# Kernel optimization log

Hardware: AMD Instinct MI355X
Metric: run time of the kernel (lower is better)

## Reference

```python
import jax, jax.numpy as jnp
import numpy as np

H, W = 512, 512
CHUNK = 128            # gaussians blended per scan step
BLUR = 0.3             # antialiasing dilation (as in 3DGS EWA low-pass)
ALPHA_MIN = 1.0 / 255.0
ALPHA_MAX = 0.99


def setup_inputs() -> dict:
    key = jax.random.key(0)
    k = jax.random.split(key, 6)
    N = 8192
    means2D = jax.random.uniform(k[0], (N, 2), jnp.float32) * jnp.array([W, H], jnp.float32)
    colors = jax.random.uniform(k[1], (N, 3), jnp.float32)
    opacities = jax.random.uniform(k[2], (N, 1), jnp.float32)
    scales = jax.random.uniform(k[3], (N, 2), jnp.float32) * 15.0 + 1.0   # pixels
    rotations = jax.random.uniform(k[4], (N, 1), jnp.float32) * (2.0 * np.pi)
    depths = jax.random.uniform(k[5], (N,), jnp.float32)
    background = jnp.zeros((3,), jnp.float32)
    return dict(means2D=means2D, colors=colors, opacities=opacities,
                scales=scales, rotations=rotations, depths=depths,
                background=background)


def _rasterize(means2D, colors, opacities, scales, rotations, depths, background):
    # depth sort: front (small depth) first
    order = jnp.argsort(depths)
    m = means2D[order]                 # [N,2] (x,y)
    col = colors[order]                # [N,3]
    op = opacities[order][:, 0]        # [N]
    s = scales[order]                  # [N,2]
    th = rotations[order][:, 0]        # [N]

    # 2D covariance  Sigma = R diag(s^2) R^T
    c, si = jnp.cos(th), jnp.sin(th)
    sx2, sy2 = s[:, 0] ** 2, s[:, 1] ** 2
    A = c * c * sx2 + si * si * sy2
    Cc = si * si * sx2 + c * c * sy2
    B = c * si * (sx2 - sy2)
    det = A * Cc - B * B
    # antialiasing: dilate covariance, compensate opacity
    A2, C2 = A + BLUR, Cc + BLUR
    det2 = A2 * C2 - B * B
    op = op * jnp.sqrt(jnp.maximum(det / det2, 0.0))
    invdet = 1.0 / det2
    ia, ib, ic = C2 * invdet, -B * invdet, A2 * invdet   # Sigma^-1 entries

    # pixel centers
    ys, xs = jnp.meshgrid(jnp.arange(H, dtype=jnp.float32) + 0.5,
                          jnp.arange(W, dtype=jnp.float32) + 0.5, indexing='ij')

    N = m.shape[0]
    nchunk = N // CHUNK
    chunk = lambda a: a.reshape((nchunk, CHUNK) + a.shape[1:])
    gs = (chunk(m), chunk(col), chunk(op), chunk(ia), chunk(ib), chunk(ic))

    def step(carry, g):
        T, acc = carry                       # T:[H,W] transmittance, acc:[3,H,W]
        gm, gcol, gop, gia, gib, gic = g     # per-chunk [C,...]
        dx = xs[None] - gm[:, 0, None, None]                 # [C,H,W]
        dy = ys[None] - gm[:, 1, None, None]
        power = (-0.5 * (gia[:, None, None] * dx * dx + gic[:, None, None] * dy * dy)
                 - gib[:, None, None] * dx * dy)
        alpha = jnp.minimum(ALPHA_MAX, gop[:, None, None] * jnp.exp(power))
        alpha = jnp.where(alpha < ALPHA_MIN, 0.0, alpha)     # skip tiny splats (as CUDA)
        one_m = 1.0 - alpha
        cum = jnp.cumprod(one_m, axis=0)                     # inclusive
        Twithin = jnp.concatenate([jnp.ones_like(cum[:1]), cum[:-1]], 0)  # exclusive
        w = alpha * Twithin * T[None]                        # blend weight per gaussian
        acc = acc + jnp.einsum('nc,nhw->chw', gcol, w)
        T = T * cum[-1]
        return (T, acc), None

    init = (jnp.ones((H, W), jnp.float32), jnp.zeros((3, H, W), jnp.float32))
    (T, acc), _ = jax.lax.scan(step, init, gs)
    color = acc + background[:, None, None] * T[None]        # [3,H,W]
    return color


def reference(means2D, colors, opacities, scales, rotations, depths, background):
    return _rasterize(means2D, colors, opacities, scales, rotations, depths, background)
```

## Files before the change

kernel.cpp:

```cpp
#include <hip/hip_runtime.h>
#include <hip/hip_fp16.h>
#include <stdint.h>

#define HH 512
#define WW 512
#define NPIX (HH*WW)
#define ALPHA_MIN_C (1.0f/255.0f)
#define ALPHA_MAX_C 0.99f
#define BLUR_C 0.3f
#define TERM_EPS 1.0e-4f
#define LOG2E 1.4426950408889634f

#define JSL 512
__global__ __launch_bounds__(256) void rank_kernel(const float* __restrict__ depths,
                                                   int N, int* __restrict__ partial) {
    __shared__ uint32_t sk[JSL];
    const int tid = threadIdx.x;
    const int ngb = N >> 8;
    const int gb = blockIdx.x % ngb;
    const int jb = blockIdx.x / ngb;
    const int j0 = jb * JSL;
    for (int i = tid; i < JSL; i += 256)
        sk[i] = __float_as_uint(depths[j0 + i]);
    __syncthreads();
    const int g = gb * 256 + tid;
    const uint32_t mb = __float_as_uint(depths[g]);
    const int glim = g - j0;
    int cnt = 0;
    const uint4* sk4 = (const uint4*)sk;
#pragma unroll 8
    for (int q = 0; q < JSL / 4; ++q) {
        uint4 v = sk4[q];
        const int i4 = q * 4;
        cnt += (v.x < mb) || (v.x == mb && (i4 + 0) < glim);
        cnt += (v.y < mb) || (v.y == mb && (i4 + 1) < glim);
        cnt += (v.z < mb) || (v.z == mb && (i4 + 2) < glim);
        cnt += (v.w < mb) || (v.w == mb && (i4 + 3) < glim);
    }
    partial[jb * N + g] = cnt;
}

__global__ __launch_bounds__(256) void prep_kernel(
    const float* __restrict__ means, const float* __restrict__ colors,
    const float* __restrict__ ops, const float* __restrict__ scales,
    const float* __restrict__ rots, const int* __restrict__ partial, int N,
    float4* __restrict__ pP, float4* __restrict__ pQ) {
    int g = blockIdx.x * 256 + threadIdx.x;
    if (g >= N) return;
    int pos = 0;
#pragma unroll
    for (int s = 0; s < 16; ++s) pos += partial[s * N + g];
    float mx = means[2*g], my = means[2*g+1];
    float th = rots[g];
    float c = cosf(th), si = sinf(th);
    float sx = scales[2*g], sy = scales[2*g+1];
    float sx2 = sx*sx, sy2 = sy*sy;
    float A  = c*c*sx2 + si*si*sy2;
    float Cc = si*si*sx2 + c*c*sy2;
    float B  = c*si*(sx2 - sy2);
    float det = A*Cc - B*B;
    float A2 = A + BLUR_C, C2 = Cc + BLUR_C;
    float det2 = A2*C2 - B*B;
    float op = ops[g] * sqrtf(fmaxf(det/det2, 0.0f));
    float invd = 1.0f/det2;
    float ia = C2*invd, ib = -B*invd, ic = A2*invd;
    float iaF = -0.5f*LOG2E*ia, icF = -0.5f*LOG2E*ic, ibF = -LOG2E*ib;
    float mid = 0.5f*(A2+C2);
    float lam = mid + sqrtf(fmaxf(mid*mid - det2, 0.0f));
    float r2;
    if (op < ALPHA_MIN_C) {
        r2 = -1.0f;
    } else {
        float t = __logf(op * 255.0f);
        r2 = fmaxf(2.0f * lam * t, 0.0f) * 1.0001f + 0.25f;
    }
    __half2 h2 = __floats2half2_rn(ibF, icF);
    unsigned ibic; __builtin_memcpy(&ibic, &h2, 4);
    unsigned r10 = __float2uint_rn(fminf(colors[3*g  ], 1.0f) * 1023.0f);
    unsigned g10 = __float2uint_rn(fminf(colors[3*g+1], 1.0f) * 1023.0f);
    unsigned b10 = __float2uint_rn(fminf(colors[3*g+2], 1.0f) * 1023.0f);
    unsigned rgb = r10 | (g10 << 10) | (b10 << 20);
    pP[pos] = make_float4(mx, my, r2, op);
    pQ[pos] = make_float4(iaF, __uint_as_float(ibic), __uint_as_float(rgb), 0.0f);
}

#define NSEG 8
#define SEGG 1024
#define CHK  128
#define NCHK (SEGG/CHK)

__device__ __forceinline__ uint2 packAT(float r, float g, float b, float t) {
    __half2 hrg = __floats2half2_rn(r, g);
    __half2 hbt = __floats2half2_rn(b, t);
    uint2 u;
    __builtin_memcpy(&u.x, &hrg, 4);
    __builtin_memcpy(&u.y, &hbt, 4);
    return u;
}

__global__ __launch_bounds__(64) void seg_blend_kernel(
    const float4* __restrict__ pP, const float4* __restrict__ pQ,
    uint2* __restrict__ segbuf) {
    __shared__ __align__(16) float sG[2][CHK*8];
    const int lane = threadIdx.x;
    const int tile = blockIdx.x & 1023;
    const int seg  = blockIdx.x >> 10;
    const int tX = tile & 31, tY = tile >> 5;
    const int px = tX*16 + (lane & 15);
    const int py = tY*16 + (lane >> 4);
    const float fx = px + 0.5f, fy = py + 0.5f;
    const float x0 = tX*16 + 0.5f, x1 = x0 + 15.0f;
    const float y0 = tY*16 + 0.5f, y1 = y0 + 15.0f;
    const uint64_t lm = (1ull << lane) - 1ull;
    float T0=1.f,T1=1.f,T2=1.f,T3=1.f;
    float aR0=0.f,aG0=0.f,aB0=0.f;
    float aR1=0.f,aG1=0.f,aB1=0.f;
    float aR2=0.f,aG2=0.f,aB2=0.f;
    float aR3=0.f,aG3=0.f,aB3=0.f;
    const int gb = seg * SEGG;

    float4 a0 = pP[gb+lane],    q0 = pQ[gb+lane];
    float4 a1 = pP[gb+64+lane], q1 = pQ[gb+64+lane];
    int cntA = 0, cntB = 0;
    {
        float nx = fminf(fmaxf(a0.x,x0),x1)-a0.x, ny = fminf(fmaxf(a0.y,y0),y1)-a0.y;
        bool f0 = (nx*nx + ny*ny) <= a0.z;
        nx = fminf(fmaxf(a1.x,x0),x1)-a1.x; ny = fminf(fmaxf(a1.y,y0),y1)-a1.y;
        bool f1 = (nx*nx + ny*ny) <= a1.z;
        uint64_t m0 = __ballot(f0);
        if (f0) { float* rec = &sG[0][__popcll(m0 & lm)*8];
                  *(float4*)rec = make_float4(a0.x,a0.y,q0.x,q0.y);
                  *(float2*)(rec+4) = make_float2(a0.w,q0.z); }
        int c0 = (int)__popcll(m0);
        uint64_t m1 = __ballot(f1);
        if (f1) { float* rec = &sG[0][(c0 + __popcll(m1 & lm))*8];
                  *(float4*)rec = make_float4(a1.x,a1.y,q1.x,q1.y);
                  *(float2*)(rec+4) = make_float2(a1.w,q1.z); }
        cntA = c0 + (int)__popcll(m1);
    }
    {   const int g = gb + CHK + lane;
        a0 = pP[g]; q0 = pQ[g]; a1 = pP[g+64]; q1 = pQ[g+64]; }

    int cur = 0;
    for (int k = 0; k < NCHK; ++k) {
        const int nxt = cur ^ 1;
        if (k + 1 < NCHK) {
            float nx = fminf(fmaxf(a0.x,x0),x1)-a0.x, ny = fminf(fmaxf(a0.y,y0),y1)-a0.y;
            bool f0 = (nx*nx + ny*ny) <= a0.z;
            nx = fminf(fmaxf(a1.x,x0),x1)-a1.x; ny = fminf(fmaxf(a1.y,y0),y1)-a1.y;
            bool f1 = (nx*nx + ny*ny) <= a1.z;
            uint64_t m0 = __ballot(f0);
            if (f0) { float* rec = &sG[nxt][__popcll(m0 & lm)*8];
                      *(float4*)rec = make_float4(a0.x,a0.y,q0.x,q0.y);
                      *(float2*)(rec+4) = make_float2(a0.w,q0.z); }
            int c0 = (int)__popcll(m0);
            uint64_t m1 = __ballot(f1);
            if (f1) { float* rec = &sG[nxt][(c0 + __popcll(m1 & lm))*8];
                      *(float4*)rec = make_float4(a1.x,a1.y,q1.x,q1.y);
                      *(float2*)(rec+4) = make_float2(a1.w,q1.z); }
            const int cn = c0 + (int)__popcll(m1);
            if (nxt == 0) cntA = cn; else cntB = cn;
            if (k + 2 < NCHK) {
                const int g = gb + (k+2)*CHK + lane;
                a0 = pP[g]; q0 = pQ[g]; a1 = pP[g+64]; q1 = pQ[g+64];
            }
        }
        const int cnt = (cur == 0) ? cntA : cntB;
        const float* segp = sG[cur];
        for (int i = 0; i < cnt; ++i) {
            const float4 r0 = *(const float4*)(segp + i*8);
            const float2 r1 = *(const float2*)(segp + i*8 + 4);
            float dx = fx - r0.x;
            float dy = fy - r0.y;
            unsigned hh = __float_as_uint(r0.w);
            __half2 h2; __builtin_memcpy(&h2, &hh, 4);
            float ibv = __half2float(h2.x);
            float icv = __half2float(h2.y);
            float bse = r0.z * (dx*dx);
            float pb  = ibv * dx;
            float d1 = dy + 4.0f, d2 = dy + 8.0f, d3 = dy + 12.0f;
            float p0 = fmaf(icv, dy*dy, fmaf(pb, dy, bse));
            float p1 = fmaf(icv, d1*d1, fmaf(pb, d1, bse));
            float p2 = fmaf(icv, d2*d2, fmaf(pb, d2, bse));
            float p3 = fmaf(icv, d3*d3, fmaf(pb, d3, bse));
            float al0 = fminf(ALPHA_MAX_C, r1.x * exp2f(p0));
            float al1 = fminf(ALPHA_MAX_C, r1.x * exp2f(p1));
            float al2 = fminf(ALPHA_MAX_C, r1.x * exp2f(p2));
            float al3 = fminf(ALPHA_MAX_C, r1.x * exp2f(p3));
            al0 = (al0 >= ALPHA_MIN_C) ? al0 : 0.0f;
            al1 = (al1 >= ALPHA_MIN_C) ? al1 : 0.0f;
            al2 = (al2 >= ALPHA_MIN_C) ? al2 : 0.0f;
            al3 = (al3 >= ALPHA_MIN_C) ? al3 : 0.0f;
            if (__any((al0 > 0.f) | (al1 > 0.f) | (al2 > 0.f) | (al3 > 0.f))) {
                unsigned rgb = __float_as_uint(r1.y);
                float cr = (float)(rgb & 1023u)         * (1.0f/1023.0f);
                float cg = (float)((rgb >> 10) & 1023u) * (1.0f/1023.0f);
                float cb = (float)((rgb >> 20) & 1023u) * (1.0f/1023.0f);
                float s0 = al0*T0, s1 = al1*T1, s2 = al2*T2, s3 = al3*T3;
                aR0 = fmaf(cr,s0,aR0); aG0 = fmaf(cg,s0,aG0); aB0 = fmaf(cb,s0,aB0);
                aR1 = fmaf(cr,s1,aR1); aG1 = fmaf(cg,s1,aG1); aB1 = fmaf(cb,s1,aB1);
                aR2 = fmaf(cr,s2,aR2); aG2 = fmaf(cg,s2,aG2); aB2 = fmaf(cb,s2,aB2);
                aR3 = fmaf(cr,s3,aR3); aG3 = fmaf(cg,s3,aG3); aB3 = fmaf(cb,s3,aB3);
                T0 = fmaf(-al0,T0,T0); T1 = fmaf(-al1,T1,T1);
                T2 = fmaf(-al2,T2,T2); T3 = fmaf(-al3,T3,T3);
            }
        }
        if (__all((T0 < TERM_EPS) & (T1 < TERM_EPS) &
                  (T2 < TERM_EPS) & (T3 < TERM_EPS))) break;
        cur = nxt;
    }
    const int pix0 = py*WW + px;
    uint2* sb = segbuf + seg * NPIX;
    sb[pix0        ] = packAT(aR0, aG0, aB0, T0);
    sb[pix0 +  4*WW] = packAT(aR1, aG1, aB1, T1);
    sb[pix0 +  8*WW] = packAT(aR2, aG2, aB2, T2);
    sb[pix0 + 12*WW] = packAT(aR3, aG3, aB3, T3);
}

__global__ __launch_bounds__(256) void composite_kernel(
    const uint2* __restrict__ segbuf, const float* __restrict__ bg,
    float* __restrict__ out) {
    const int pix = blockIdx.x * 256 + threadIdx.x;
    float R = 0.f, G = 0.f, B = 0.f, T = 1.f;
#pragma unroll
    for (int s = 0; s < NSEG; ++s) {
        uint2 v = segbuf[s * NPIX + pix];
        __half2 hrg, hbt;
        __builtin_memcpy(&hrg, &v.x, 4);
        __builtin_memcpy(&hbt, &v.y, 4);
        R = fmaf(T, __half2float(hrg.x), R);
        G = fmaf(T, __half2float(hrg.y), G);
        B = fmaf(T, __half2float(hbt.x), B);
        T *= __half2float(hbt.y);
    }
    out[pix]          = R + bg[0]*T;
    out[pix +   NPIX] = G + bg[1]*T;
    out[pix + 2*NPIX] = B + bg[2]*T;
}

extern "C" void kernel_launch(void* const* d_in, const int* in_sizes, int n_in,
                              void* d_out, int out_size, void* d_ws, size_t ws_size,
                              hipStream_t stream) {
    const float* means   = (const float*)d_in[0];
    const float* colors  = (const float*)d_in[1];
    const float* ops     = (const float*)d_in[2];
    const float* scales  = (const float*)d_in[3];
    const float* rots    = (const float*)d_in[4];
    const float* depths  = (const float*)d_in[5];
    const float* bg      = (const float*)d_in[6];
    const int N = in_sizes[0] / 2;

    char* ws = (char*)d_ws;
    float4* pP    = (float4*)(ws);
    float4* pQ    = (float4*)(ws + (size_t)N*16);
    int*    part  = (int*)  (ws + (size_t)N*32);
    uint2*  segb  = (uint2*)(ws + (size_t)N*32 + (size_t)16*N*4);

    const int ngb = N / 256;
    const int njb = N / JSL;
    rank_kernel<<<dim3(ngb*njb), dim3(256), 0, stream>>>(depths, N, part);
    prep_kernel<<<dim3((N+255)/256), dim3(256), 0, stream>>>(
        means, colors, ops, scales, rots, part, N, pP, pQ);
    seg_blend_kernel<<<dim3(NSEG*1024), dim3(64), 0, stream>>>(pP, pQ, segb);
    composite_kernel<<<dim3(NPIX/256), dim3(256), 0, stream>>>(
        segb, bg, (float*)d_out);
}
```

Before: 136.6 us.

## Use per-axis ellipse bounding box culling and fold log-opacity into exponent

The preprocess now stores per-axis half-extents of the alpha-threshold ellipse instead of a circular radius from the largest eigenvalue. The tile test becomes an axis-aligned box overlap, which is tighter for elongated or rotated splats and so sends fewer gaussians to the per-pixel blend loop. Log2 of opacity is folded into the exponent so each of the four alpha evaluations loses a multiply, and the blend loop is unrolled by two. The tighter bound depends on the half-extent formula being conservative; if it is not, visible splats could be culled.

```diff
diff --git a/kernel.cpp b/kernel.cpp
--- a/kernel.cpp
+++ b/kernel.cpp
@@ -65,14 +65,14 @@
     float invd = 1.0f/det2;
     float ia = C2*invd, ib = -B*invd, ic = A2*invd;
     float iaF = -0.5f*LOG2E*ia, icF = -0.5f*LOG2E*ic, ibF = -LOG2E*ib;
-    float mid = 0.5f*(A2+C2);
-    float lam = mid + sqrtf(fmaxf(mid*mid - det2, 0.0f));
-    float r2;
+    float bx, by, lop;
     if (op < ALPHA_MIN_C) {
-        r2 = -1.0f;
+        bx = -1.0f; by = -1.0f; lop = -128.0f;
     } else {
         float t = __logf(op * 255.0f);
-        r2 = fmaxf(2.0f * lam * t, 0.0f) * 1.0001f + 0.25f;
+        bx = sqrtf(fmaxf(2.0f * t * A2, 0.0f)) * 1.0001f + 0.1f;
+        by = sqrtf(fmaxf(2.0f * t * C2, 0.0f)) * 1.0001f + 0.1f;
+        lop = __log2f(op);
     }
     __half2 h2 = __floats2half2_rn(ibF, icF);
     unsigned ibic; __builtin_memcpy(&ibic, &h2, 4);
@@ -80,8 +80,8 @@
     unsigned g10 = __float2uint_rn(fminf(colors[3*g+1], 1.0f) * 1023.0f);
     unsigned b10 = __float2uint_rn(fminf(colors[3*g+2], 1.0f) * 1023.0f);
     unsigned rgb = r10 | (g10 << 10) | (b10 << 20);
-    pP[pos] = make_float4(mx, my, r2, op);
-    pQ[pos] = make_float4(iaF, __uint_as_float(ibic), __uint_as_float(rgb), 0.0f);
+    pP[pos] = make_float4(mx, my, bx, by);
+    pQ[pos] = make_float4(iaF, __uint_as_float(ibic), __uint_as_float(rgb), lop);
 }
 
 #define NSEG 8
@@ -123,19 +123,21 @@
     float4 a1 = pP[gb+64+lane], q1 = pQ[gb+64+lane];
     int cntA = 0, cntB = 0;
     {
-        float nx = fminf(fmaxf(a0.x,x0),x1)-a0.x, ny = fminf(fmaxf(a0.y,y0),y1)-a0.y;
-        bool f0 = (nx*nx + ny*ny) <= a0.z;
-        nx = fminf(fmaxf(a1.x,x0),x1)-a1.x; ny = fminf(fmaxf(a1.y,y0),y1)-a1.y;
-        bool f1 = (nx*nx + ny*ny) <= a1.z;
+        float nx = fabsf(fminf(fmaxf(a0.x,x0),x1)-a0.x);
+        float ny = fabsf(fminf(fmaxf(a0.y,y0),y1)-a0.y);
+        bool f0 = (nx <= a0.z) & (ny <= a0.w);
+        nx = fabsf(fminf(fmaxf(a1.x,x0),x1)-a1.x);
+        ny = fabsf(fminf(fmaxf(a1.y,y0),y1)-a1.y);
+        bool f1 = (nx <= a1.z) & (ny <= a1.w);
         uint64_t m0 = __ballot(f0);
         if (f0) { float* rec = &sG[0][__popcll(m0 & lm)*8];
                   *(float4*)rec = make_float4(a0.x,a0.y,q0.x,q0.y);
-                  *(float2*)(rec+4) = make_float2(a0.w,q0.z); }
+                  *(float2*)(rec+4) = make_float2(q0.w,q0.z); }
         int c0 = (int)__popcll(m0);
         uint64_t m1 = __ballot(f1);
         if (f1) { float* rec = &sG[0][(c0 + __popcll(m1 & lm))*8];
                   *(float4*)rec = make_float4(a1.x,a1.y,q1.x,q1.y);
-                  *(float2*)(rec+4) = make_float2(a1.w,q1.z); }
+                  *(float2*)(rec+4) = make_float2(q1.w,q1.z); }
         cntA = c0 + (int)__popcll(m1);
     }
     {   const int g = gb + CHK + lane;
@@ -145,19 +147,21 @@
     for (int k = 0; k < NCHK; ++k) {
         const int nxt = cur ^ 1;
         if (k + 1 < NCHK) {
-            float nx = fminf(fmaxf(a0.x,x0),x1)-a0.x, ny = fminf(fmaxf(a0.y,y0),y1)-a0.y;
-            bool f0 = (nx*nx + ny*ny) <= a0.z;
-            nx = fminf(fmaxf(a1.x,x0),x1)-a1.x; ny = fminf(fmaxf(a1.y,y0),y1)-a1.y;
-            bool f1 = (nx*nx + ny*ny) <= a1.z;
+            float nx = fabsf(fminf(fmaxf(a0.x,x0),x1)-a0.x);
+            float ny = fabsf(fminf(fmaxf(a0.y,y0),y1)-a0.y);
+            bool f0 = (nx <= a0.z) & (ny <= a0.w);
+            nx = fabsf(fminf(fmaxf(a1.x,x0),x1)-a1.x);
+            ny = fabsf(fminf(fmaxf(a1.y,y0),y1)-a1.y);
+            bool f1 = (nx <= a1.z) & (ny <= a1.w);
             uint64_t m0 = __ballot(f0);
             if (f0) { float* rec = &sG[nxt][__popcll(m0 & lm)*8];
                       *(float4*)rec = make_float4(a0.x,a0.y,q0.x,q0.y);
-                      *(float2*)(rec+4) = make_float2(a0.w,q0.z); }
+                      *(float2*)(rec+4) = make_float2(q0.w,q0.z); }
             int c0 = (int)__popcll(m0);
             uint64_t m1 = __ballot(f1);
             if (f1) { float* rec = &sG[nxt][(c0 + __popcll(m1 & lm))*8];
                       *(float4*)rec = make_float4(a1.x,a1.y,q1.x,q1.y);
-                      *(float2*)(rec+4) = make_float2(a1.w,q1.z); }
+                      *(float2*)(rec+4) = make_float2(q1.w,q1.z); }
             const int cn = c0 + (int)__popcll(m1);
             if (nxt == 0) cntA = cn; else cntB = cn;
             if (k + 2 < NCHK) {
@@ -167,6 +171,7 @@
         }
         const int cnt = (cur == 0) ? cntA : cntB;
         const float* segp = sG[cur];
+#pragma unroll 2
         for (int i = 0; i < cnt; ++i) {
             const float4 r0 = *(const float4*)(segp + i*8);
             const float2 r1 = *(const float2*)(segp + i*8 + 4);
@@ -176,17 +181,17 @@
             __half2 h2; __builtin_memcpy(&h2, &hh, 4);
             float ibv = __half2float(h2.x);
             float icv = __half2float(h2.y);
-            float bse = r0.z * (dx*dx);
+            float bse = fmaf(r0.z, dx*dx, r1.x);
             float pb  = ibv * dx;
             float d1 = dy + 4.0f, d2 = dy + 8.0f, d3 = dy + 12.0f;
             float p0 = fmaf(icv, dy*dy, fmaf(pb, dy, bse));
             float p1 = fmaf(icv, d1*d1, fmaf(pb, d1, bse));
             float p2 = fmaf(icv, d2*d2, fmaf(pb, d2, bse));
             float p3 = fmaf(icv, d3*d3, fmaf(pb, d3, bse));
-            float al0 = fminf(ALPHA_MAX_C, r1.x * exp2f(p0));
-            float al1 = fminf(ALPHA_MAX_C, r1.x * exp2f(p1));
-            float al2 = fminf(ALPHA_MAX_C, r1.x * exp2f(p2));
-            float al3 = fminf(ALPHA_MAX_C, r1.x * exp2f(p3));
+            float al0 = fminf(ALPHA_MAX_C, exp2f(p0));
+            float al1 = fminf(ALPHA_MAX_C, exp2f(p1));
+            float al2 = fminf(ALPHA_MAX_C, exp2f(p2));
+            float al3 = fminf(ALPHA_MAX_C, exp2f(p3));
             al0 = (al0 >= ALPHA_MIN_C) ? al0 : 0.0f;
             al1 = (al1 >= ALPHA_MIN_C) ? al1 : 0.0f;
             al2 = (al2 >= ALPHA_MIN_C) ? al2 : 0.0f;
```

Result: faster. 133.4 us (-2.4%).
